# Performance work log

Measured on AMD Instinct MI355X. Metric: run time of the kernel, lower is better.

## Reference

```python
import jax, jax.numpy as jnp
import numpy as np

NEG_INF = -1e9  # additive mask value (every row attends to itself, so softmax is safe)


def setup_inputs() -> dict:
    D, H, N = 256, 8, 4096
    key = jax.random.key(0)
    ks = jax.random.split(key, 7)
    slots = jax.random.normal(ks[0], (1, N, D), dtype=jnp.float32)
    batch_idx = jnp.sort(jax.random.randint(ks[1], (N,), 0, 16)).astype(jnp.int32)
    s_in = 1.0 / np.sqrt(D)
    w_in = jax.random.uniform(ks[2], (3 * D, D), jnp.float32, -s_in, s_in)
    b_in = jnp.zeros((3 * D,), jnp.float32)
    w_out = jax.random.uniform(ks[3], (D, D), jnp.float32, -s_in, s_in)
    b_out = jnp.zeros((D,), jnp.float32)
    ln_gamma = jnp.ones((D,), jnp.float32)
    ln_beta = jnp.zeros((D,), jnp.float32)
    return {"slots": slots, "batch_idx": batch_idx, "w_in": w_in, "b_in": b_in,
            "w_out": w_out, "b_out": b_out, "ln_gamma": ln_gamma, "ln_beta": ln_beta}


def _mha_block_diag(x, batch_idx, w_in, b_in, w_out, b_out, num_heads):
    # x: [N, D]
    N, D = x.shape
    hd = D // num_heads
    qkv = x @ w_in.T + b_in                      # [N, 3D]
    q, k, v = jnp.split(qkv, 3, axis=-1)
    q = q.reshape(N, num_heads, hd).transpose(1, 0, 2)   # [H, N, hd]
    k = k.reshape(N, num_heads, hd).transpose(1, 0, 2)
    v = v.reshape(N, num_heads, hd).transpose(1, 0, 2)
    scale = 1.0 / np.sqrt(hd)
    scores = jnp.einsum('hnd,hmd->hnm', q, k) * scale    # [H, N, N]
    mask = batch_idx[:, None] != batch_idx[None, :]      # True = blocked
    scores = jnp.where(mask[None], NEG_INF, scores)
    attn = jax.nn.softmax(scores, axis=-1)
    out = jnp.einsum('hnm,hmd->hnd', attn, v)            # [H, N, hd]
    out = out.transpose(1, 0, 2).reshape(N, D)
    return out @ w_out.T + b_out


def _layer_norm(x, gamma, beta, eps=1e-5):
    mu = jnp.mean(x, axis=-1, keepdims=True)
    var = jnp.mean(jnp.square(x - mu), axis=-1, keepdims=True)
    return (x - mu) * jax.lax.rsqrt(var + eps) * gamma + beta


def reference(slots, batch_idx, w_in, b_in, w_out, b_out, ln_gamma, ln_beta):
    # slots: [1, N, D]; dropout prob is 0.0 (eval-mode reference)
    x = slots[0]
    delta = _mha_block_diag(x, batch_idx, w_in, b_in, w_out, b_out, num_heads=8)
    out = _layer_norm(x + delta, ln_gamma, ln_beta)
    return out[None]
```

## Files before the change

kernel.cpp:

```cpp
#include <hip/hip_runtime.h>
#include <hip/hip_bf16.h>

#define NROWS 4096
#define DMODEL 256
#define NHEADS 8
#define HD 32

typedef __attribute__((ext_vector_type(8))) short short8;
typedef __attribute__((ext_vector_type(4))) float f32x4;

__global__ __launch_bounds__(256) void prep_kernel(
    const float* __restrict__ slots, const float* __restrict__ w_in,
    const float* __restrict__ w_out, const int* __restrict__ bidx,
    __hip_bfloat16* __restrict__ Abf, __hip_bfloat16* __restrict__ Winb,
    __hip_bfloat16* __restrict__ Woutb, int* __restrict__ segs) {
  const int bid = blockIdx.x;
  const float* src;
  __hip_bfloat16* dst;
  int i;
  if (bid < 1024)      { src = slots; dst = Abf;   i = (bid * 256 + (int)threadIdx.x) * 4; }
  else if (bid < 1216) { src = w_in;  dst = Winb;  i = ((bid - 1024) * 256 + (int)threadIdx.x) * 4; }
  else if (bid < 1280) { src = w_out; dst = Woutb; i = ((bid - 1216) * 256 + (int)threadIdx.x) * 4; }
  else {
    const int r = (bid - 1280) * 256 + threadIdx.x;
    const int b = bidx[r];
    if (r == 0 || bidx[r - 1] != b) segs[b] = r;
    if (r == NROWS - 1 || bidx[r + 1] != b) segs[16 + b] = r + 1;
    return;
  }
  const float4 v = *(const float4*)(src + i);
  __hip_bfloat162 lo, hi;
  lo.x = __float2bfloat16(v.x); lo.y = __float2bfloat16(v.y);
  hi.x = __float2bfloat16(v.z); hi.y = __float2bfloat16(v.w);
  *(__hip_bfloat162*)(dst + i) = lo;
  *(__hip_bfloat162*)(dst + i + 2) = hi;
}

__global__ __launch_bounds__(256, 4) void gemm_qkv(
    const __hip_bfloat16* __restrict__ A,
    const __hip_bfloat16* __restrict__ B,
    const float* __restrict__ bias,
    __hip_bfloat16* __restrict__ Qo,
    __hip_bfloat16* __restrict__ Ko,
    __hip_bfloat16* __restrict__ Vo) {
  const int wv   = threadIdx.x >> 6;
  const int lane = threadIdx.x & 63;
  const int lo16 = lane & 15;
  const int quad = lane >> 4;
  const int bm = blockIdx.y * 64 + wv * 16;
  const int bn = blockIdx.x * 64;

  f32x4 acc[4] = {};
  #pragma unroll
  for (int k0 = 0; k0 < 256; k0 += 32) {
    const short8 af = *(const short8*)(A + (size_t)(bm + lo16) * 256 + k0 + quad * 8);
    #pragma unroll
    for (int ni = 0; ni < 4; ni++) {
      const short8 bf = *(const short8*)(B + (size_t)(bn + ni * 16 + lo16) * 256 + k0 + quad * 8);
      acc[ni] = __builtin_amdgcn_mfma_f32_16x16x32_bf16(af, bf, acc[ni], 0, 0, 0);
    }
  }
  #pragma unroll
  for (int ni = 0; ni < 4; ni++) {
    const int col = bn + ni * 16 + lo16;
    const int sel = col >> 8;
    const int h = (col & 255) >> 5;
    const int d = col & 31;
    const float bv = bias[col];
    #pragma unroll
    for (int r = 0; r < 4; r++) {
      const int n = bm + quad * 4 + r;
      const __hip_bfloat16 v = __float2bfloat16(acc[ni][r] + bv);
      if (sel == 0)      Qo[((size_t)h * NROWS + n) * HD + d] = v;
      else if (sel == 1) Ko[((size_t)h * NROWS + n) * HD + d] = v;
      else               Vo[((size_t)h * HD + d) * NROWS + n] = v;
    }
  }
}

__global__ __launch_bounds__(256, 4) void attn_mfma(
    const __hip_bfloat16* __restrict__ Qb,
    const __hip_bfloat16* __restrict__ Kb,
    const __hip_bfloat16* __restrict__ Vt,
    const int* __restrict__ bidx,
    const int* __restrict__ segs,
    __hip_bfloat16* __restrict__ out)
{
  __shared__ __align__(16) __hip_bfloat16 Plds_all[4][16][40];
  __shared__ float mld[4][16], lld[4][16];
  __shared__ float Old[4][16][32];
  const int wv   = threadIdx.x >> 6;
  const int lane = threadIdx.x & 63;
  const int qt   = blockIdx.x >> 3;
  const int h    = blockIdx.x & 7;
  const int r0   = qt * 16;
  const int lo16 = lane & 15;
  const int quad = lane >> 4;
  __hip_bfloat16 (*Plds)[40] = Plds_all[wv];

  int st[4], en[4];
  #pragma unroll
  for (int r = 0; r < 4; r++) {
    const int b = bidx[r0 + quad * 4 + r];
    st[r] = segs[b];
    en[r] = segs[16 + b];
  }
  const int kstart = segs[bidx[r0]] & ~31;
  const int kend   = segs[16 + bidx[r0 + 15]];
  const int ntiles = (kend - kstart + 31) >> 5;

  const short8 qf = *(const short8*)(Qb + ((size_t)h * NROWS + r0 + lo16) * HD + quad * 8);

  f32x4 o0 = {0.f, 0.f, 0.f, 0.f}, o1 = {0.f, 0.f, 0.f, 0.f};
  float m[4], l[4];
  #pragma unroll
  for (int r = 0; r < 4; r++) { m[r] = -1e30f; l[r] = 0.0f; }

  const float scale = 0.17677669529663687f;

  for (int t = wv; t < ntiles; t += 4) {
    const int c0 = kstart + t * 32;
    const int col0 = c0 + lo16;
    const int col1 = col0 + 16;
    const int colc0 = min(col0, NROWS - 1);
    const int colc1 = min(col1, NROWS - 1);
    const short8 kf0 = *(const short8*)(Kb + ((size_t)h * NROWS + colc0) * HD + quad * 8);
    const short8 kf1 = *(const short8*)(Kb + ((size_t)h * NROWS + colc1) * HD + quad * 8);
    const int vc = min(c0 + quad * 8, NROWS - 8);
    const short8 vf0 = *(const short8*)(Vt + ((size_t)h * HD + lo16) * NROWS + vc);
    const short8 vf1 = *(const short8*)(Vt + ((size_t)h * HD + 16 + lo16) * NROWS + vc);

    const f32x4 z = {0.f, 0.f, 0.f, 0.f};
    f32x4 s0 = __builtin_amdgcn_mfma_f32_16x16x32_bf16(qf, kf0, z, 0, 0, 0);
    f32x4 s1 = __builtin_amdgcn_mfma_f32_16x16x32_bf16(qf, kf1, z, 0, 0, 0);

    #pragma unroll
    for (int r = 0; r < 4; r++) {
      const bool ok0 = (col0 >= st[r]) & (col0 < en[r]);
      const bool ok1 = (col1 >= st[r]) & (col1 < en[r]);
      const float sc0 = ok0 ? s0[r] * scale : -1e30f;
      const float sc1 = ok1 ? s1[r] * scale : -1e30f;
      float mx = fmaxf(sc0, sc1);
      mx = fmaxf(mx, __shfl_xor(mx, 1));
      mx = fmaxf(mx, __shfl_xor(mx, 2));
      mx = fmaxf(mx, __shfl_xor(mx, 4));
      mx = fmaxf(mx, __shfl_xor(mx, 8));
      const float nm = fmaxf(m[r], mx);
      const float alpha = __expf(m[r] - nm);
      const float p0 = ok0 ? __expf(sc0 - nm) : 0.0f;
      const float p1 = ok1 ? __expf(sc1 - nm) : 0.0f;
      float ps = p0 + p1;
      ps += __shfl_xor(ps, 1);
      ps += __shfl_xor(ps, 2);
      ps += __shfl_xor(ps, 4);
      ps += __shfl_xor(ps, 8);
      l[r] = l[r] * alpha + ps;
      m[r] = nm;
      o0[r] *= alpha;
      o1[r] *= alpha;
      Plds[quad * 4 + r][lo16]      = __float2bfloat16(p0);
      Plds[quad * 4 + r][lo16 + 16] = __float2bfloat16(p1);
    }
    const short8 pf = *(const short8*)&Plds[lo16][quad * 8];
    o0 = __builtin_amdgcn_mfma_f32_16x16x32_bf16(pf, vf0, o0, 0, 0, 0);
    o1 = __builtin_amdgcn_mfma_f32_16x16x32_bf16(pf, vf1, o1, 0, 0, 0);
  }

  #pragma unroll
  for (int r = 0; r < 4; r++) {
    const int row = quad * 4 + r;
    Old[wv][row][lo16]      = o0[r];
    Old[wv][row][lo16 + 16] = o1[r];
    if (lo16 == 0) { mld[wv][row] = m[r]; lld[wv][row] = l[r]; }
  }
  __syncthreads();

  const int row = threadIdx.x >> 4;
  const int c   = threadIdx.x & 15;
  float M = fmaxf(fmaxf(mld[0][row], mld[1][row]),
                  fmaxf(mld[2][row], mld[3][row]));
  float L = 0.f, O0 = 0.f, O1 = 0.f;
  #pragma unroll
  for (int w = 0; w < 4; w++) {
    const float e = __expf(mld[w][row] - M);
    L  += e * lld[w][row];
    O0 += e * Old[w][row][c];
    O1 += e * Old[w][row][c + 16];
  }
  const float inv = 1.0f / L;
  const int grow = r0 + row;
  out[(size_t)grow * DMODEL + h * HD + c]      = __float2bfloat16(O0 * inv);
  out[(size_t)grow * DMODEL + h * HD + 16 + c] = __float2bfloat16(O1 * inv);
}

__global__ __launch_bounds__(256, 4) void gemm_out_ln(
    const __hip_bfloat16* __restrict__ A,
    const __hip_bfloat16* __restrict__ B,
    const float* __restrict__ bias,
    const float* __restrict__ x,
    const float* __restrict__ gamma, const float* __restrict__ beta,
    float* __restrict__ out) {
  __shared__ float red1[16][4], red2[16][4];
  const int wv   = threadIdx.x >> 6;
  const int lane = threadIdx.x & 63;
  const int lo16 = lane & 15;
  const int quad = lane >> 4;
  const int r0 = blockIdx.x * 16;
  const int wn = wv * 64;

  f32x4 acc[4] = {};
  #pragma unroll
  for (int k0 = 0; k0 < 256; k0 += 32) {
    const short8 af = *(const short8*)(A + (size_t)(r0 + lo16) * 256 + k0 + quad * 8);
    #pragma unroll
    for (int ni = 0; ni < 4; ni++) {
      const short8 bf = *(const short8*)(B + (size_t)(wn + ni * 16 + lo16) * 256 + k0 + quad * 8);
      acc[ni] = __builtin_amdgcn_mfma_f32_16x16x32_bf16(af, bf, acc[ni], 0, 0, 0);
    }
  }

  float val[4][4];
  float s1[4] = {}, s2[4] = {};
  #pragma unroll
  for (int ni = 0; ni < 4; ni++) {
    const int col = wn + ni * 16 + lo16;
    const float bv = bias[col];
    #pragma unroll
    for (int r = 0; r < 4; r++) {
      const int row = r0 + quad * 4 + r;
      const float v = acc[ni][r] + bv + x[(size_t)row * DMODEL + col];
      val[ni][r] = v;
      s1[r] += v;
      s2[r] += v * v;
    }
  }
  #pragma unroll
  for (int r = 0; r < 4; r++) {
    #pragma unroll
    for (int off = 1; off < 16; off <<= 1) {
      s1[r] += __shfl_xor(s1[r], off);
      s2[r] += __shfl_xor(s2[r], off);
    }
    if (lo16 == 0) { red1[quad * 4 + r][wv] = s1[r]; red2[quad * 4 + r][wv] = s2[r]; }
  }
  __syncthreads();
  #pragma unroll
  for (int r = 0; r < 4; r++) {
    const int lrow = quad * 4 + r;
    const float mean = (red1[lrow][0] + red1[lrow][1] + red1[lrow][2] + red1[lrow][3]) * (1.0f / DMODEL);
    const float ex2  = (red2[lrow][0] + red2[lrow][1] + red2[lrow][2] + red2[lrow][3]) * (1.0f / DMODEL);
    const float rstd = rsqrtf(fmaxf(ex2 - mean * mean, 0.0f) + 1e-5f);
    const int row = r0 + lrow;
    #pragma unroll
    for (int ni = 0; ni < 4; ni++) {
      const int col = wn + ni * 16 + lo16;
      out[(size_t)row * DMODEL + col] =
          (val[ni][r] - mean) * rstd * gamma[col] + beta[col];
    }
  }
}

extern "C" void kernel_launch(void* const* d_in, const int* in_sizes, int n_in,
                              void* d_out, int out_size, void* d_ws, size_t ws_size,
                              hipStream_t stream) {
  const float* slots  = (const float*)d_in[0];
  const int*   bidx   = (const int*)  d_in[1];
  const float* w_in   = (const float*)d_in[2];
  const float* b_in   = (const float*)d_in[3];
  const float* w_out  = (const float*)d_in[4];
  const float* b_out  = (const float*)d_in[5];
  const float* ln_g   = (const float*)d_in[6];
  const float* ln_b   = (const float*)d_in[7];
  float* out = (float*)d_out;

  char* ws = (char*)d_ws;
  __hip_bfloat16* Abf   = (__hip_bfloat16*)(ws);
  __hip_bfloat16* Qb    = (__hip_bfloat16*)(ws + (2u  << 20));
  __hip_bfloat16* Kb    = (__hip_bfloat16*)(ws + (4u  << 20));
  __hip_bfloat16* Vt    = (__hip_bfloat16*)(ws + (6u  << 20));
  __hip_bfloat16* attnb = (__hip_bfloat16*)(ws + (8u  << 20));
  __hip_bfloat16* Winb  = (__hip_bfloat16*)(ws + (10u << 20));
  __hip_bfloat16* Woutb = (__hip_bfloat16*)(ws + (10u << 20) + (512u << 10));
  int*            segs  = (int*)           (ws + (11u << 20));

  prep_kernel<<<1296, 256, 0, stream>>>(slots, w_in, w_out, bidx,
                                        Abf, Winb, Woutb, segs);
  {
    dim3 grid(768 / 64, NROWS / 64);
    gemm_qkv<<<grid, 256, 0, stream>>>(Abf, Winb, b_in, Qb, Kb, Vt);
  }
  attn_mfma<<<(NROWS / 16) * NHEADS, 256, 0, stream>>>(Qb, Kb, Vt, bidx,
                                                       segs, attnb);
  gemm_out_ln<<<NROWS / 16, 256, 0, stream>>>(attnb, Woutb, b_out, slots,
                                              ln_g, ln_b, out);
}
```

Before: 116.2 us.

## Transpose QK^T MFMA so each lane owns one query row in attention softmax

Swaps the MFMA operand order so the score tile is laid out with query rows per lane, letting row max and sum reduce with two cross-quad shuffles instead of four per row. It folds log2(e) into the scale to use exp2 directly, replaces per-row segment bounds with a single unsigned range check, and skips rescaling the output accumulators when the running max is unchanged. The alpha values are passed back to the row layout through a small LDS buffer. The clamps on the K/V column indices are removed, so tiles near the end of the sequence may read past the buffers.

```diff
diff --git a/kernel.cpp b/kernel.cpp
--- a/kernel.cpp
+++ b/kernel.cpp
@@ -87,6 +87,7 @@
     __hip_bfloat16* __restrict__ out)
 {
   __shared__ __align__(16) __hip_bfloat16 Plds_all[4][16][40];
+  __shared__ __align__(16) float alds_all[4][16];
   __shared__ float mld[4][16], lld[4][16];
   __shared__ float Old[4][16][32];
   const int wv   = threadIdx.x >> 6;
@@ -97,14 +98,12 @@
   const int lo16 = lane & 15;
   const int quad = lane >> 4;
   __hip_bfloat16 (*Plds)[40] = Plds_all[wv];
-
-  int st[4], en[4];
-  #pragma unroll
-  for (int r = 0; r < 4; r++) {
-    const int b = bidx[r0 + quad * 4 + r];
-    st[r] = segs[b];
-    en[r] = segs[16 + b];
-  }
+  float* alds = alds_all[wv];
+
+  const int bq  = bidx[r0 + lo16];
+  const int stq = segs[bq];
+  const unsigned rng = (unsigned)(segs[16 + bq] - stq);
+
   const int kstart = segs[bidx[r0]] & ~31;
   const int kend   = segs[16 + bidx[r0 + 15]];
   const int ntiles = (kend - kstart + 31) >> 5;
@@ -112,54 +111,64 @@
   const short8 qf = *(const short8*)(Qb + ((size_t)h * NROWS + r0 + lo16) * HD + quad * 8);
 
   f32x4 o0 = {0.f, 0.f, 0.f, 0.f}, o1 = {0.f, 0.f, 0.f, 0.f};
-  float m[4], l[4];
-  #pragma unroll
-  for (int r = 0; r < 4; r++) { m[r] = -1e30f; l[r] = 0.0f; }
-
-  const float scale = 0.17677669529663687f;
+  float m = -1e30f, l = 0.0f;
+  const float scale2 = 0.17677669529663687f * 1.4426950408889634f;
 
   for (int t = wv; t < ntiles; t += 4) {
     const int c0 = kstart + t * 32;
-    const int col0 = c0 + lo16;
-    const int col1 = col0 + 16;
-    const int colc0 = min(col0, NROWS - 1);
-    const int colc1 = min(col1, NROWS - 1);
-    const short8 kf0 = *(const short8*)(Kb + ((size_t)h * NROWS + colc0) * HD + quad * 8);
-    const short8 kf1 = *(const short8*)(Kb + ((size_t)h * NROWS + colc1) * HD + quad * 8);
-    const int vc = min(c0 + quad * 8, NROWS - 8);
+    const short8 kf0 = *(const short8*)(Kb + ((size_t)h * NROWS + c0 + lo16) * HD + quad * 8);
+    const short8 kf1 = *(const short8*)(Kb + ((size_t)h * NROWS + c0 + 16 + lo16) * HD + quad * 8);
+    const int vc = c0 + quad * 8;
     const short8 vf0 = *(const short8*)(Vt + ((size_t)h * HD + lo16) * NROWS + vc);
     const short8 vf1 = *(const short8*)(Vt + ((size_t)h * HD + 16 + lo16) * NROWS + vc);
 
     const f32x4 z = {0.f, 0.f, 0.f, 0.f};
-    f32x4 s0 = __builtin_amdgcn_mfma_f32_16x16x32_bf16(qf, kf0, z, 0, 0, 0);
-    f32x4 s1 = __builtin_amdgcn_mfma_f32_16x16x32_bf16(qf, kf1, z, 0, 0, 0);
-
+    f32x4 s0 = __builtin_amdgcn_mfma_f32_16x16x32_bf16(kf0, qf, z, 0, 0, 0);
+    f32x4 s1 = __builtin_amdgcn_mfma_f32_16x16x32_bf16(kf1, qf, z, 0, 0, 0);
+
+    const int kb = c0 + quad * 4 - stq;
+    float p0v[4], p1v[4];
+    float mx = -3e38f;
     #pragma unroll
     for (int r = 0; r < 4; r++) {
-      const bool ok0 = (col0 >= st[r]) & (col0 < en[r]);
-      const bool ok1 = (col1 >= st[r]) & (col1 < en[r]);
-      const float sc0 = ok0 ? s0[r] * scale : -1e30f;
-      const float sc1 = ok1 ? s1[r] * scale : -1e30f;
-      float mx = fmaxf(sc0, sc1);
-      mx = fmaxf(mx, __shfl_xor(mx, 1));
-      mx = fmaxf(mx, __shfl_xor(mx, 2));
-      mx = fmaxf(mx, __shfl_xor(mx, 4));
-      mx = fmaxf(mx, __shfl_xor(mx, 8));
-      const float nm = fmaxf(m[r], mx);
-      const float alpha = __expf(m[r] - nm);
-      const float p0 = ok0 ? __expf(sc0 - nm) : 0.0f;
-      const float p1 = ok1 ? __expf(sc1 - nm) : 0.0f;
-      float ps = p0 + p1;
-      ps += __shfl_xor(ps, 1);
-      ps += __shfl_xor(ps, 2);
-      ps += __shfl_xor(ps, 4);
-      ps += __shfl_xor(ps, 8);
-      l[r] = l[r] * alpha + ps;
-      m[r] = nm;
-      o0[r] *= alpha;
-      o1[r] *= alpha;
-      Plds[quad * 4 + r][lo16]      = __float2bfloat16(p0);
-      Plds[quad * 4 + r][lo16 + 16] = __float2bfloat16(p1);
+      const float sc0 = ((unsigned)(kb + r)      < rng) ? s0[r] * scale2 : -3e38f;
+      const float sc1 = ((unsigned)(kb + 16 + r) < rng) ? s1[r] * scale2 : -3e38f;
+      p0v[r] = sc0; p1v[r] = sc1;
+      mx = fmaxf(mx, fmaxf(sc0, sc1));
+    }
+    mx = fmaxf(mx, __shfl_xor(mx, 16));
+    mx = fmaxf(mx, __shfl_xor(mx, 32));
+    const float nm = fmaxf(m, mx);
+    float ps = 0.0f;
+    #pragma unroll
+    for (int r = 0; r < 4; r++) {
+      p0v[r] = __builtin_amdgcn_exp2f(p0v[r] - nm);
+      p1v[r] = __builtin_amdgcn_exp2f(p1v[r] - nm);
+      ps += p0v[r] + p1v[r];
+    }
+    ps += __shfl_xor(ps, 16);
+    ps += __shfl_xor(ps, 32);
+
+    const float alpha = __builtin_amdgcn_exp2f(m - nm);
+    l = l * alpha + ps;
+    if (!__all(nm == m)) {
+      if (quad == 0) alds[lo16] = alpha;
+      const f32x4 av = *(const f32x4*)&alds[quad * 4];
+      #pragma unroll
+      for (int r = 0; r < 4; r++) { o0[r] *= av[r]; o1[r] *= av[r]; }
+    }
+    m = nm;
+
+    {
+      __hip_bfloat162* pw0 = (__hip_bfloat162*)&Plds[lo16][quad * 4];
+      __hip_bfloat162* pw1 = (__hip_bfloat162*)&Plds[lo16][16 + quad * 4];
+      __hip_bfloat162 a, b;
+      a.x = __float2bfloat16(p0v[0]); a.y = __float2bfloat16(p0v[1]);
+      b.x = __float2bfloat16(p0v[2]); b.y = __float2bfloat16(p0v[3]);
+      pw0[0] = a; pw0[1] = b;
+      a.x = __float2bfloat16(p1v[0]); a.y = __float2bfloat16(p1v[1]);
+      b.x = __float2bfloat16(p1v[2]); b.y = __float2bfloat16(p1v[3]);
+      pw1[0] = a; pw1[1] = b;
     }
     const short8 pf = *(const short8*)&Plds[lo16][quad * 8];
     o0 = __builtin_amdgcn_mfma_f32_16x16x32_bf16(pf, vf0, o0, 0, 0, 0);
@@ -171,8 +180,8 @@
     const int row = quad * 4 + r;
     Old[wv][row][lo16]      = o0[r];
     Old[wv][row][lo16 + 16] = o1[r];
-    if (lo16 == 0) { mld[wv][row] = m[r]; lld[wv][row] = l[r]; }
-  }
+  }
+  if (quad == 0) { mld[wv][lo16] = m; lld[wv][lo16] = l; }
   __syncthreads();
 
   const int row = threadIdx.x >> 4;
@@ -182,7 +191,7 @@
   float L = 0.f, O0 = 0.f, O1 = 0.f;
   #pragma unroll
   for (int w = 0; w < 4; w++) {
-    const float e = __expf(mld[w][row] - M);
+    const float e = __builtin_amdgcn_exp2f(mld[w][row] - M);
     L  += e * lld[w][row];
     O0 += e * Old[w][row][c];
     O1 += e * Old[w][row][c + 16];
```

Result: faster. 113.0 us (-2.8%).
